# Performance work log

Hardware: AMD Instinct MI355X
Metric: run time of the kernel (lower is better)

## Reference

```python
import jax, jax.numpy as jnp
import numpy as np

N_NODES = 100000   # number of atoms in the (batched) molecular graph
N_EDGES = 1600000  # directed edges (avg degree 16)
F_DIM = 128        # featureSize
P_DIM = 2048       # fingerPrintLength
RADIUS = 4


def setup_inputs() -> dict:
    key = jax.random.key(0)
    k1, k2, k3, k4, k5 = jax.random.split(key, 5)
    atomsFeatures = jax.random.normal(k1, (N_NODES, F_DIM), dtype=jnp.float32)
    edge_src = jax.random.randint(k2, (N_EDGES,), 0, N_NODES, dtype=jnp.int32)
    edge_dst = jax.random.randint(k3, (N_EDGES,), 0, N_NODES, dtype=jnp.int32)
    W1 = jax.random.normal(k4, (F_DIM, F_DIM), dtype=jnp.float32) / np.float32(np.sqrt(F_DIM))
    b1 = jnp.zeros((F_DIM,), dtype=jnp.float32)
    W2 = jax.random.normal(k5, (F_DIM, P_DIM), dtype=jnp.float32) / np.float32(np.sqrt(F_DIM))
    b2 = jnp.zeros((P_DIM,), dtype=jnp.float32)
    return {"atomsFeatures": atomsFeatures, "W1": W1, "b1": b1,
            "W2": W2, "b2": b2, "edge_src": edge_src, "edge_dst": edge_dst}


def reference(atomsFeatures, W1, b1, W2, b2, edge_src, edge_dst):
    # Duvenaud neural fingerprint:
    # for r in range(radius):
    #   agg[i]  = x[i] + sum_{j in N(i)} x[j]          (gather + segment-sum)
    #   h       = relu(agg @ W1 + b1)                  (lin1)
    #   fp     += sum_i softmax(h @ W2 + b2)           (lin2 + softmax scatter-add)
    #   x       = h
    x = atomsFeatures
    fp = jnp.zeros((1, W2.shape[1]), dtype=x.dtype)
    for _ in range(RADIUS):
        neigh = jax.ops.segment_sum(x[edge_src], edge_dst, num_segments=N_NODES)
        agg = x + neigh                                    # [N, F]
        h = jax.nn.relu(agg @ W1 + b1)                     # [N, F]
        logits = h @ W2 + b2                               # [N, P]
        fp = fp + jnp.sum(jax.nn.softmax(logits, axis=-1), axis=0, keepdims=True)
        x = h
    return fp
```

## Files before the change

kernel.cpp:

```cpp
#include <hip/hip_runtime.h>
#include <hip/hip_bf16.h>
#include <cstdint>
#include <cstddef>

#define F_DIM 128
#define P_DIM 2048
#define RADIUS 4
#define HT_STRIDE 136
#define LOG2E 1.4426950408889634f

typedef short s16x8 __attribute__((ext_vector_type(8)));
typedef float f32x4 __attribute__((ext_vector_type(4)));
typedef float f32x2 __attribute__((ext_vector_type(2)));

static __device__ __forceinline__ float bf2f(ushort u) {
    union { float f; uint i; } v; v.i = ((uint)u) << 16; return v.f;
}
static __device__ __forceinline__ ushort f2bf(float f) {
    uint u = __float_as_uint(f);
    uint r = (u + 0x7fffu + ((u >> 16) & 1u)) >> 16;
    return (ushort)r;
}
static __device__ __forceinline__ f32x2 bfpair(uint u) {
    union { float f; uint i; } lo, hi;
    lo.i = u << 16; hi.i = u & 0xffff0000u;
    f32x2 r; r.x = lo.f; r.y = hi.f; return r;
}
static __device__ __forceinline__ f32x4 mfma16(s16x8 a, s16x8 b, f32x4 c) {
    return __builtin_amdgcn_mfma_f32_16x16x32_bf16(a, b, c, 0, 0, 0);
}
static __device__ __forceinline__ float ex2(float x) { return __builtin_amdgcn_exp2f(x); }
static __device__ __forceinline__ float lg2(float x) { return __builtin_amdgcn_logf(x); }


__global__ void hist_kernel(const int* __restrict__ dst, int* __restrict__ counts, int E) {
    int e = blockIdx.x * blockDim.x + threadIdx.x;
    if (e < E) atomicAdd(&counts[dst[e]], 1);
}

__global__ __launch_bounds__(1024) void scan1_kernel(const int* __restrict__ counts,
                                                     int* __restrict__ offs,
                                                     int* __restrict__ partials, int N) {
    __shared__ int buf[2][1024];
    int i = (blockIdx.x << 10) + threadIdx.x;
    int v = (i < N) ? counts[i] : 0;
    int src = 0;
    buf[0][threadIdx.x] = v;
    __syncthreads();
    for (int off = 1; off < 1024; off <<= 1) {
        int d = src ^ 1;
        int val = buf[src][threadIdx.x];
        if (threadIdx.x >= (unsigned)off) val += buf[src][threadIdx.x - off];
        buf[d][threadIdx.x] = val;
        src = d;
        __syncthreads();
    }
    int inc = buf[src][threadIdx.x];
    if (i < N) offs[i + 1] = inc;
    if (threadIdx.x == 1023) partials[blockIdx.x] = inc;
}

__global__ __launch_bounds__(1024) void scan2_kernel(int* __restrict__ partials, int nb) {
    __shared__ int buf[2][1024];
    int t = threadIdx.x;
    int v = (t < nb) ? partials[t] : 0;
    int src = 0;
    buf[0][t] = v;
    __syncthreads();
    for (int off = 1; off < 1024; off <<= 1) {
        int d = src ^ 1;
        int val = buf[src][t];
        if (t >= (unsigned)off) val += buf[src][t - off];
        buf[d][t] = val;
        src = d;
        __syncthreads();
    }
    if (t < nb) partials[t] = (t == 0) ? 0 : buf[src][t - 1];
}

__global__ void scan3_kernel(int* __restrict__ offs, const int* __restrict__ partials, int N) {
    int i = blockIdx.x * blockDim.x + threadIdx.x;
    if (i < N) offs[i + 1] += partials[i >> 10];
    if (i == 0) offs[0] = 0;
}

__global__ void copy_kernel(const int* __restrict__ offs, int* __restrict__ cursor, int N) {
    int i = blockIdx.x * blockDim.x + threadIdx.x;
    if (i < N) cursor[i] = offs[i];
}

__global__ void scatter_kernel(const int* __restrict__ src, const int* __restrict__ dst,
                               int* __restrict__ cursor, int* __restrict__ srcs_sorted, int E) {
    int e = blockIdx.x * blockDim.x + threadIdx.x;
    if (e < E) {
        int d = dst[e];
        int pos = atomicAdd(&cursor[d], 1);
        srcs_sorted[pos] = src[e];
    }
}


__global__ void cvt_bf16_kernel(const float* __restrict__ src, ushort* __restrict__ dst, int n) {
    int i = blockIdx.x * blockDim.x + threadIdx.x;
    if (i < n) dst[i] = f2bf(src[i]);
}

__global__ void scale_kernel(const float* __restrict__ src, float* __restrict__ dst,
                             int n, float scale) {
    int i = blockIdx.x * blockDim.x + threadIdx.x;
    if (i < n) dst[i] = src[i] * scale;
}

__global__ void swizzle_split_kernel(const float* __restrict__ src, ushort* __restrict__ dst,
                                     int P, int total, float scale) {
    int d = blockIdx.x * blockDim.x + threadIdx.x;
    if (d >= total) return;
    int j    = d & 7;
    int lane = (d >> 3) & 63;
    int s    = (d >> 9) & 1;
    int kt   = (d >> 10) & 3;
    int pt   = d >> 12;
    int k = kt * 32 + (lane >> 4) * 8 + j;
    int p = pt * 16 + (lane & 15);
    float w = src[k * P + p] * scale;
    ushort hi = f2bf(w);
    ushort out = hi;
    if (s) out = f2bf(w - bf2f(hi));
    dst[d] = out;
}


#define ACC8(acc2, u) { \
    acc2[0] += bfpair(u.x); acc2[1] += bfpair(u.y); \
    acc2[2] += bfpair(u.z); acc2[3] += bfpair(u.w); }

__global__ __launch_bounds__(256) void agg_kernel(const ushort* __restrict__ x,
                                                  const int* __restrict__ offs,
                                                  const int* __restrict__ srcs,
                                                  ushort* __restrict__ agg, int N) {
    int wid = (blockIdx.x * blockDim.x + threadIdx.x) >> 6;
    int lane = threadIdx.x & 63;
    int q = lane >> 4;
    int l16 = lane & 15;
    int n0 = wid * 8 + q;
    int n1 = wid * 8 + 4 + q;
    const uint4* xr = (const uint4*)x;

    f32x2 accA[4], accB[4];
    #pragma unroll
    for (int i = 0; i < 4; ++i) { accA[i] = (f32x2){0.f, 0.f}; accB[i] = (f32x2){0.f, 0.f}; }
    int eA = 0, eA1 = 0, eB = 0, eB1 = 0;
    if (n0 < N) {
        uint4 v = xr[(size_t)n0 * 16 + l16];
        ACC8(accA, v);
        eA = offs[n0]; eA1 = offs[n0 + 1];
    }
    if (n1 < N) {
        uint4 v = xr[(size_t)n1 * 16 + l16];
        ACC8(accB, v);
        eB = offs[n1]; eB1 = offs[n1 + 1];
    }
    while (eA + 2 <= eA1 && eB + 2 <= eB1) {
        int ja0 = srcs[eA], ja1 = srcs[eA + 1]; eA += 2;
        int jb0 = srcs[eB], jb1 = srcs[eB + 1]; eB += 2;
        uint4 ua0 = xr[(size_t)ja0 * 16 + l16];
        uint4 ua1 = xr[(size_t)ja1 * 16 + l16];
        uint4 ub0 = xr[(size_t)jb0 * 16 + l16];
        uint4 ub1 = xr[(size_t)jb1 * 16 + l16];
        ACC8(accA, ua0); ACC8(accA, ua1);
        ACC8(accB, ub0); ACC8(accB, ub1);
    }
    while (eA < eA1 && eB < eB1) {
        int ja = srcs[eA++];
        int jb = srcs[eB++];
        uint4 ua = xr[(size_t)ja * 16 + l16];
        uint4 ub = xr[(size_t)jb * 16 + l16];
        ACC8(accA, ua);
        ACC8(accB, ub);
    }
    while (eA < eA1) {
        int ja = srcs[eA++];
        uint4 ua = xr[(size_t)ja * 16 + l16];
        ACC8(accA, ua);
    }
    while (eB < eB1) {
        int jb = srcs[eB++];
        uint4 ub = xr[(size_t)jb * 16 + l16];
        ACC8(accB, ub);
    }
    if (n0 < N) {
        uint4 o;
        o.x = ((uint)f2bf(accA[0].y) << 16) | (uint)f2bf(accA[0].x);
        o.y = ((uint)f2bf(accA[1].y) << 16) | (uint)f2bf(accA[1].x);
        o.z = ((uint)f2bf(accA[2].y) << 16) | (uint)f2bf(accA[2].x);
        o.w = ((uint)f2bf(accA[3].y) << 16) | (uint)f2bf(accA[3].x);
        ((uint4*)agg)[(size_t)n0 * 16 + l16] = o;
    }
    if (n1 < N) {
        uint4 o;
        o.x = ((uint)f2bf(accB[0].y) << 16) | (uint)f2bf(accB[0].x);
        o.y = ((uint)f2bf(accB[1].y) << 16) | (uint)f2bf(accB[1].x);
        o.z = ((uint)f2bf(accB[2].y) << 16) | (uint)f2bf(accB[2].x);
        o.w = ((uint)f2bf(accB[3].y) << 16) | (uint)f2bf(accB[3].x);
        ((uint4*)agg)[(size_t)n1 * 16 + l16] = o;
    }
}


#define LOADB(bb_) { _Pragma("unroll") for (int f = 0; f < 8; ++f) bb_[f] = wpn[f * 64]; wpn += 512; }

#define MFMA4(cc, bb_) { \
    _Pragma("unroll") for (int g = 0; g < 4; ++g) cc[g] = mfma16(a[g][0], bb_[0], czero); \
    _Pragma("unroll") for (int g = 0; g < 4; ++g) cc[g] = mfma16(a[g][0], bb_[1], cc[g]); \
    _Pragma("unroll") for (int kt = 1; kt < 4; ++kt) { \
        _Pragma("unroll") for (int g = 0; g < 4; ++g) cc[g] = mfma16(a[g][kt], bb_[kt * 2 + 0], cc[g]); \
        _Pragma("unroll") for (int g = 0; g < 4; ++g) cc[g] = mfma16(a[g][kt], bb_[kt * 2 + 1], cc[g]); } }

#define P1_UPD4(cc, bbv) { \
    f32x2 bb2; bb2.x = (bbv); bb2.y = (bbv); \
    _Pragma("unroll") for (int g = 0; g < 4; ++g) \
    _Pragma("unroll") for (int h = 0; h < 2; ++h) { \
        int j2 = g * 2 + h; \
        f32x2 v; v.x = cc[g][2 * h]; v.y = cc[g][2 * h + 1]; \
        v = v + bb2; \
        f32x2 d = v - m2_[j2]; \
        f32x2 e; e.x = ex2(-fabsf(d.x)); e.y = ex2(-fabsf(d.y)); \
        f32x2 t1 = s2_[j2] + e; \
        f32x2 t2 = __builtin_elementwise_fma(s2_[j2], e, one2); \
        s2_[j2].x = d.x > 0.f ? t2.x : t1.x; \
        s2_[j2].y = d.y > 0.f ? t2.y : t1.y; \
        m2_[j2] = __builtin_elementwise_max(m2_[j2], v); \
    } }

#define P2_UPD4(cc, bbv, ptv) { \
    f32x2 bb2; bb2.x = (bbv); bb2.y = (bbv); \
    f32x2 tot2; tot2.x = 0.f; tot2.y = 0.f; \
    _Pragma("unroll") for (int g = 0; g < 4; ++g) \
    _Pragma("unroll") for (int h = 0; h < 2; ++h) { \
        f32x2 v; v.x = cc[g][2 * h]; v.y = cc[g][2 * h + 1]; \
        v = v + bb2 + bbk2[g * 2 + h]; \
        tot2.x += ex2(v.x); tot2.y += ex2(v.y); \
    } \
    float tot = tot2.x + tot2.y; \
    tot += __shfl_xor(tot, 16); \
    tot += __shfl_xor(tot, 32); \
    if (lane < 16) atomicAdd(&fp[(ptv) * 16 + lane], tot); }

__global__ __launch_bounds__(256, 2) void round_kernel(
        const ushort* __restrict__ agg,
        const ushort* __restrict__ w1sw,
        const float*  __restrict__ b1,
        const ushort* __restrict__ w2sw,
        const float*  __restrict__ b2l,
        ushort* __restrict__ h_out,
        float* __restrict__ fp,
        int N) {
    __shared__ ushort smem_u[64 * HT_STRIDE];
    ushort* hT = smem_u;
    float* mbuf = (float*)smem_u;
    float* sbuf = ((float*)smem_u) + 256;

    const int tid = threadIdx.x;
    const int w = tid >> 6;
    const int lane = tid & 63;
    const int q = lane >> 4;
    const int l15 = lane & 15;
    const int nodeBase = blockIdx.x * 64;
    const int ptBase = w * 32;

    const f32x4 czero = {0.f, 0.f, 0.f, 0.f};
    f32x2 one2; one2.x = 1.0f; one2.y = 1.0f;

    const s16x8* w1v = (const s16x8*)w1sw;
    const s16x8* w2v = (const s16x8*)w2sw;

    s16x8 a[4][4];
    #pragma unroll
    for (int g = 0; g < 4; ++g) {
        int node = nodeBase + g * 16 + l15;
        #pragma unroll
        for (int kt = 0; kt < 4; ++kt) {
            if (node < N)
                a[g][kt] = *(const s16x8*)(agg + (size_t)node * F_DIM + kt * 32 + q * 8);
            else
                a[g][kt] = (s16x8){0, 0, 0, 0, 0, 0, 0, 0};
        }
    }

    #pragma unroll
    for (int t = 0; t < 2; ++t) {
        int pt = 2 * w + t;
        f32x4 c[4];
        const s16x8* wp = w1v + pt * 8 * 64;
        {
            s16x8 bh = wp[0 * 64 + lane];
            s16x8 bl = wp[1 * 64 + lane];
            #pragma unroll
            for (int g = 0; g < 4; ++g) {
                c[g] = mfma16(a[g][0], bh, czero);
                c[g] = mfma16(a[g][0], bl, c[g]);
            }
        }
        #pragma unroll
        for (int kt = 1; kt < 4; ++kt) {
            s16x8 bh = wp[(kt * 2 + 0) * 64 + lane];
            s16x8 bl = wp[(kt * 2 + 1) * 64 + lane];
            #pragma unroll
            for (int g = 0; g < 4; ++g) {
                c[g] = mfma16(a[g][kt], bh, c[g]);
                c[g] = mfma16(a[g][kt], bl, c[g]);
            }
        }
        float bb = b1[pt * 16 + l15];
        #pragma unroll
        for (int g = 0; g < 4; ++g)
            #pragma unroll
            for (int r = 0; r < 4; ++r) {
                float v = c[g][r] + bb;
                v = v > 0.f ? v : 0.f;
                hT[(g * 16 + q * 4 + r) * HT_STRIDE + pt * 16 + l15] = f2bf(v);
            }
    }
    __syncthreads();

    #pragma unroll
    for (int it = 0; it < 4; ++it) {
        int idx = it * 256 + tid;
        int row = idx >> 4;
        int chunk = idx & 15;
        int gnode = nodeBase + row;
        if (gnode < N) {
            s16x8 vv = *(const s16x8*)&hT[row * HT_STRIDE + chunk * 8];
            *(s16x8*)(h_out + (size_t)gnode * F_DIM + chunk * 8) = vv;
        }
    }

    #pragma unroll
    for (int g = 0; g < 4; ++g)
        #pragma unroll
        for (int kt = 0; kt < 4; ++kt)
            a[g][kt] = *(const s16x8*)&hT[(g * 16 + l15) * HT_STRIDE + kt * 32 + q * 8];
    __syncthreads();

    f32x2 m2_[8], s2_[8];
    #pragma unroll
    for (int j = 0; j < 8; ++j) {
        m2_[j].x = -INFINITY; m2_[j].y = -INFINITY;
        s2_[j].x = 0.f;       s2_[j].y = 0.f;
    }

    {
        const s16x8* wpn = w2v + ptBase * 8 * 64 + lane;
        const float* bpn = b2l + ptBase * 16 + l15;
        s16x8 bA[8], bB[8];
        f32x4 cA[4], cB[4];
        float bbA, bbB;
        LOADB(bA); bbA = *bpn; bpn += 16;
        LOADB(bB); bbB = *bpn; bpn += 16;
        MFMA4(cA, bA);
        #pragma unroll 1
        for (int k = 0; k < 15; ++k) {
            float bbu = bbA;
            LOADB(bA); bbA = *bpn; bpn += 16;
            MFMA4(cB, bB);
            P1_UPD4(cA, bbu);
            float bbv = bbB;
            LOADB(bB); bbB = *bpn; bpn += 16;
            MFMA4(cA, bA);
            P1_UPD4(cB, bbv);
        }
        MFMA4(cB, bB);
        P1_UPD4(cA, bbA);
        P1_UPD4(cB, bbB);
    }

    #pragma unroll
    for (int j = 0; j < 16; ++j) {
        int j2 = (j >> 2) * 2 + ((j >> 1) & 1);
        int cmp = j & 1;
        float mm = m2_[j2][cmp], ss = s2_[j2][cmp];
        #pragma unroll
        for (int off = 1; off <= 8; off <<= 1) {
            float om = __shfl_xor(mm, off);
            float os = __shfl_xor(ss, off);
            float nm = fmaxf(mm, om);
            ss = ss * ex2(mm - nm) + os * ex2(om - nm);
            mm = nm;
        }
        if (l15 == 0) {
            int node = (j >> 2) * 16 + q * 4 + (j & 3);
            mbuf[node * 4 + w] = mm;
            sbuf[node * 4 + w] = ss;
        }
    }
    __syncthreads();

    f32x2 bbk2[8];
    #pragma unroll
    for (int j = 0; j < 16; ++j) {
        int node = (j >> 2) * 16 + q * 4 + (j & 3);
        float4 mv = *(const float4*)&mbuf[node * 4];
        float4 sv = *(const float4*)&sbuf[node * 4];
        float nm = fmaxf(fmaxf(mv.x, mv.y), fmaxf(mv.z, mv.w));
        float ss = sv.x * ex2(mv.x - nm) + sv.y * ex2(mv.y - nm)
                 + sv.z * ex2(mv.z - nm) + sv.w * ex2(mv.w - nm);
        float bb = (nodeBase + node < N) ? (-nm - lg2(ss)) : -INFINITY;
        int j2 = (j >> 2) * 2 + ((j >> 1) & 1);
        bbk2[j2][j & 1] = bb;
    }

    {
        const s16x8* wpn = w2v + ptBase * 8 * 64 + lane;
        const float* bpn = b2l + ptBase * 16 + l15;
        s16x8 bA[8], bB[8];
        f32x4 cA[4], cB[4];
        float bbA, bbB;
        LOADB(bA); bbA = *bpn; bpn += 16;
        LOADB(bB); bbB = *bpn; bpn += 16;
        MFMA4(cA, bA);
        #pragma unroll 1
        for (int k = 0; k < 15; ++k) {
            float bbu = bbA;
            LOADB(bA); bbA = *bpn; bpn += 16;
            MFMA4(cB, bB);
            P2_UPD4(cA, bbu, ptBase + 2 * k);
            float bbv = bbB;
            LOADB(bB); bbB = *bpn; bpn += 16;
            MFMA4(cA, bA);
            P2_UPD4(cB, bbv, ptBase + 2 * k + 1);
        }
        MFMA4(cB, bB);
        P2_UPD4(cA, bbA, ptBase + 30);
        P2_UPD4(cB, bbB, ptBase + 31);
    }
}


extern "C" void kernel_launch(void* const* d_in, const int* in_sizes, int n_in,
                              void* d_out, int out_size, void* d_ws, size_t ws_size,
                              hipStream_t stream) {
    const float* atoms = (const float*)d_in[0];
    const float* W1    = (const float*)d_in[1];
    const float* b1    = (const float*)d_in[2];
    const float* W2    = (const float*)d_in[3];
    const float* b2    = (const float*)d_in[4];
    const int* esrc    = (const int*)d_in[5];
    const int* edst    = (const int*)d_in[6];
    float* fp          = (float*)d_out;
    const int N = in_sizes[0] / F_DIM;
    const int E = in_sizes[5];

    char* ws = (char*)d_ws;
    ushort* xA   = (ushort*)ws;  ws += (size_t)N * F_DIM * sizeof(ushort);
    ushort* xB   = (ushort*)ws;  ws += (size_t)N * F_DIM * sizeof(ushort);
    ushort* aggb = (ushort*)ws;  ws += (size_t)N * F_DIM * sizeof(ushort);
    ushort* w1sw = (ushort*)ws;  ws += (size_t)F_DIM * F_DIM * 2 * sizeof(ushort);
    ushort* w2sw = (ushort*)ws;  ws += (size_t)F_DIM * P_DIM * 2 * sizeof(ushort);
    float*  b2l  = (float*)ws;   ws += (size_t)P_DIM * sizeof(float);
    int* offs    = (int*)ws;     ws += (((size_t)(N + 1) * sizeof(int) + 255) & ~255ull);
    int* cursor  = (int*)ws;     ws += (((size_t)N * sizeof(int) + 255) & ~255ull);
    int* partials = (int*)ws;    ws += 4096;
    int* srcs    = (int*)ws;

    hipMemsetAsync(d_out, 0, (size_t)out_size * sizeof(float), stream);
    hipMemsetAsync(cursor, 0, (size_t)N * sizeof(int), stream);

    int eb = (E + 255) / 256;
    hist_kernel<<<eb, 256, 0, stream>>>(edst, cursor, E);
    int nb1 = (N + 1023) >> 10;
    scan1_kernel<<<nb1, 1024, 0, stream>>>(cursor, offs, partials, N);
    scan2_kernel<<<1, 1024, 0, stream>>>(partials, nb1);
    scan3_kernel<<<(N + 255) / 256, 256, 0, stream>>>(offs, partials, N);
    copy_kernel<<<(N + 255) / 256, 256, 0, stream>>>(offs, cursor, N);
    scatter_kernel<<<eb, 256, 0, stream>>>(esrc, edst, cursor, srcs, E);

    int nconv = N * F_DIM;
    cvt_bf16_kernel<<<(nconv + 255) / 256, 256, 0, stream>>>(atoms, xA, nconv);
    int t1 = F_DIM * F_DIM * 2;
    swizzle_split_kernel<<<(t1 + 255) / 256, 256, 0, stream>>>(W1, w1sw, F_DIM, t1, 1.0f);
    int t2 = F_DIM * P_DIM * 2;
    swizzle_split_kernel<<<(t2 + 255) / 256, 256, 0, stream>>>(W2, w2sw, P_DIM, t2, LOG2E);
    scale_kernel<<<(P_DIM + 255) / 256, 256, 0, stream>>>(b2, b2l, P_DIM, LOG2E);

    const ushort* x = xA;
    ushort* xnext = xB;
    int rblocks = (N + 63) / 64;
    int ablocks = (N + 31) / 32;
    for (int r = 0; r < RADIUS; ++r) {
        agg_kernel<<<ablocks, 256, 0, stream>>>(x, offs, srcs, aggb, N);
        round_kernel<<<rblocks, 256, 0, stream>>>(aggb, w1sw, b1, w2sw, b2l,
                                                  xnext, fp, N);
        x = xnext;
        xnext = (xnext == xB) ? xA : xB;
    }
}
```

Measured before the change: 1.534 ms.

## Give each wave its own node rows across all P columns, dropping cross-wave softmax merge

The round kernel now assigns each wave 32 nodes over the full 2048-column output, instead of 64 nodes shared by four waves that each cover a quarter of the columns. Each wave's online-softmax stats are therefore complete, which removes the shared-memory max/sum exchange and two block barriers. Blocks grow to 128 nodes and periodic __syncthreads are added in the W2 loops, presumably to keep waves in step for cache reuse of W2. The trade-off is that each wave streams all of W2 twice, so per-wave W2 loads and atomicAdd traffic to fp rise four-fold.

```diff
diff --git a/kernel.cpp b/kernel.cpp
--- a/kernel.cpp
+++ b/kernel.cpp
@@ -209,16 +209,16 @@
 
 #define LOADB(bb_) { _Pragma("unroll") for (int f = 0; f < 8; ++f) bb_[f] = wpn[f * 64]; wpn += 512; }
 
-#define MFMA4(cc, bb_) { \
-    _Pragma("unroll") for (int g = 0; g < 4; ++g) cc[g] = mfma16(a[g][0], bb_[0], czero); \
-    _Pragma("unroll") for (int g = 0; g < 4; ++g) cc[g] = mfma16(a[g][0], bb_[1], cc[g]); \
+#define MFMA2(cc, bb_) { \
+    _Pragma("unroll") for (int g = 0; g < 2; ++g) cc[g] = mfma16(a[g][0], bb_[0], czero); \
+    _Pragma("unroll") for (int g = 0; g < 2; ++g) cc[g] = mfma16(a[g][0], bb_[1], cc[g]); \
     _Pragma("unroll") for (int kt = 1; kt < 4; ++kt) { \
-        _Pragma("unroll") for (int g = 0; g < 4; ++g) cc[g] = mfma16(a[g][kt], bb_[kt * 2 + 0], cc[g]); \
-        _Pragma("unroll") for (int g = 0; g < 4; ++g) cc[g] = mfma16(a[g][kt], bb_[kt * 2 + 1], cc[g]); } }
-
-#define P1_UPD4(cc, bbv) { \
+        _Pragma("unroll") for (int g = 0; g < 2; ++g) cc[g] = mfma16(a[g][kt], bb_[kt * 2 + 0], cc[g]); \
+        _Pragma("unroll") for (int g = 0; g < 2; ++g) cc[g] = mfma16(a[g][kt], bb_[kt * 2 + 1], cc[g]); } }
+
+#define P1_UPD2(cc, bbv) { \
     f32x2 bb2; bb2.x = (bbv); bb2.y = (bbv); \
-    _Pragma("unroll") for (int g = 0; g < 4; ++g) \
+    _Pragma("unroll") for (int g = 0; g < 2; ++g) \
     _Pragma("unroll") for (int h = 0; h < 2; ++h) { \
         int j2 = g * 2 + h; \
         f32x2 v; v.x = cc[g][2 * h]; v.y = cc[g][2 * h + 1]; \
@@ -232,10 +232,10 @@
         m2_[j2] = __builtin_elementwise_max(m2_[j2], v); \
     } }
 
-#define P2_UPD4(cc, bbv, ptv) { \
+#define P2_UPD2(cc, bbv, ptv) { \
     f32x2 bb2; bb2.x = (bbv); bb2.y = (bbv); \
     f32x2 tot2; tot2.x = 0.f; tot2.y = 0.f; \
-    _Pragma("unroll") for (int g = 0; g < 4; ++g) \
+    _Pragma("unroll") for (int g = 0; g < 2; ++g) \
     _Pragma("unroll") for (int h = 0; h < 2; ++h) { \
         f32x2 v; v.x = cc[g][2 * h]; v.y = cc[g][2 * h + 1]; \
         v = v + bb2 + bbk2[g * 2 + h]; \
@@ -255,18 +255,15 @@
         ushort* __restrict__ h_out,
         float* __restrict__ fp,
         int N) {
-    __shared__ ushort smem_u[64 * HT_STRIDE];
-    ushort* hT = smem_u;
-    float* mbuf = (float*)smem_u;
-    float* sbuf = ((float*)smem_u) + 256;
+    __shared__ ushort hT[128 * HT_STRIDE];
 
     const int tid = threadIdx.x;
     const int w = tid >> 6;
     const int lane = tid & 63;
     const int q = lane >> 4;
     const int l15 = lane & 15;
-    const int nodeBase = blockIdx.x * 64;
-    const int ptBase = w * 32;
+    const int nodeBase = blockIdx.x * 128;
+    const int rowBase = w * 32;
 
     const f32x4 czero = {0.f, 0.f, 0.f, 0.f};
     f32x2 one2; one2.x = 1.0f; one2.y = 1.0f;
@@ -274,10 +271,10 @@
     const s16x8* w1v = (const s16x8*)w1sw;
     const s16x8* w2v = (const s16x8*)w2sw;
 
-    s16x8 a[4][4];
-    #pragma unroll
-    for (int g = 0; g < 4; ++g) {
-        int node = nodeBase + g * 16 + l15;
+    s16x8 a[2][4];
+    #pragma unroll
+    for (int g = 0; g < 2; ++g) {
+        int node = nodeBase + rowBase + g * 16 + l15;
         #pragma unroll
         for (int kt = 0; kt < 4; ++kt) {
             if (node < N)
@@ -287,16 +284,15 @@
         }
     }
 
-    #pragma unroll
-    for (int t = 0; t < 2; ++t) {
-        int pt = 2 * w + t;
-        f32x4 c[4];
-        const s16x8* wp = w1v + pt * 8 * 64;
+    #pragma unroll 1
+    for (int ft = 0; ft < 8; ++ft) {
+        f32x4 c[2];
+        const s16x8* wp = w1v + ft * 8 * 64;
         {
             s16x8 bh = wp[0 * 64 + lane];
             s16x8 bl = wp[1 * 64 + lane];
             #pragma unroll
-            for (int g = 0; g < 4; ++g) {
+            for (int g = 0; g < 2; ++g) {
                 c[g] = mfma16(a[g][0], bh, czero);
                 c[g] = mfma16(a[g][0], bl, c[g]);
             }
@@ -306,76 +302,76 @@
             s16x8 bh = wp[(kt * 2 + 0) * 64 + lane];
             s16x8 bl = wp[(kt * 2 + 1) * 64 + lane];
             #pragma unroll
-            for (int g = 0; g < 4; ++g) {
+            for (int g = 0; g < 2; ++g) {
                 c[g] = mfma16(a[g][kt], bh, c[g]);
                 c[g] = mfma16(a[g][kt], bl, c[g]);
             }
         }
-        float bb = b1[pt * 16 + l15];
+        float bb = b1[ft * 16 + l15];
         #pragma unroll
-        for (int g = 0; g < 4; ++g)
+        for (int g = 0; g < 2; ++g)
             #pragma unroll
             for (int r = 0; r < 4; ++r) {
                 float v = c[g][r] + bb;
                 v = v > 0.f ? v : 0.f;
-                hT[(g * 16 + q * 4 + r) * HT_STRIDE + pt * 16 + l15] = f2bf(v);
+                hT[(rowBase + g * 16 + q * 4 + r) * HT_STRIDE + ft * 16 + l15] = f2bf(v);
             }
     }
-    __syncthreads();
-
-    #pragma unroll
-    for (int it = 0; it < 4; ++it) {
-        int idx = it * 256 + tid;
+
+    #pragma unroll
+    for (int it = 0; it < 8; ++it) {
+        int idx = it * 64 + lane;
         int row = idx >> 4;
         int chunk = idx & 15;
-        int gnode = nodeBase + row;
+        int gnode = nodeBase + rowBase + row;
         if (gnode < N) {
-            s16x8 vv = *(const s16x8*)&hT[row * HT_STRIDE + chunk * 8];
+            s16x8 vv = *(const s16x8*)&hT[(rowBase + row) * HT_STRIDE + chunk * 8];
             *(s16x8*)(h_out + (size_t)gnode * F_DIM + chunk * 8) = vv;
         }
     }
 
     #pragma unroll
-    for (int g = 0; g < 4; ++g)
+    for (int g = 0; g < 2; ++g)
         #pragma unroll
         for (int kt = 0; kt < 4; ++kt)
-            a[g][kt] = *(const s16x8*)&hT[(g * 16 + l15) * HT_STRIDE + kt * 32 + q * 8];
-    __syncthreads();
-
-    f32x2 m2_[8], s2_[8];
-    #pragma unroll
-    for (int j = 0; j < 8; ++j) {
+            a[g][kt] = *(const s16x8*)&hT[(rowBase + g * 16 + l15) * HT_STRIDE + kt * 32 + q * 8];
+
+    f32x2 m2_[4], s2_[4];
+    #pragma unroll
+    for (int j = 0; j < 4; ++j) {
         m2_[j].x = -INFINITY; m2_[j].y = -INFINITY;
         s2_[j].x = 0.f;       s2_[j].y = 0.f;
     }
 
     {
-        const s16x8* wpn = w2v + ptBase * 8 * 64 + lane;
-        const float* bpn = b2l + ptBase * 16 + l15;
+        const s16x8* wpn = w2v + lane;
+        const float* bpn = b2l + l15;
         s16x8 bA[8], bB[8];
-        f32x4 cA[4], cB[4];
+        f32x4 cA[2], cB[2];
         float bbA, bbB;
         LOADB(bA); bbA = *bpn; bpn += 16;
         LOADB(bB); bbB = *bpn; bpn += 16;
-        MFMA4(cA, bA);
+        MFMA2(cA, bA);
         #pragma unroll 1
-        for (int k = 0; k < 15; ++k) {
+        for (int k = 0; k < 63; ++k) {
             float bbu = bbA;
             LOADB(bA); bbA = *bpn; bpn += 16;
-            MFMA4(cB, bB);
-            P1_UPD4(cA, bbu);
+            MFMA2(cB, bB);
+            P1_UPD2(cA, bbu);
             float bbv = bbB;
             LOADB(bB); bbB = *bpn; bpn += 16;
-            MFMA4(cA, bA);
-            P1_UPD4(cB, bbv);
-        }
-        MFMA4(cB, bB);
-        P1_UPD4(cA, bbA);
-        P1_UPD4(cB, bbB);
-    }
-
-    #pragma unroll
-    for (int j = 0; j < 16; ++j) {
+            MFMA2(cA, bA);
+            P1_UPD2(cB, bbv);
+            if ((k & 3) == 3) __syncthreads();
+        }
+        MFMA2(cB, bB);
+        P1_UPD2(cA, bbA);
+        P1_UPD2(cB, bbB);
+    }
+
+    f32x2 bbk2[4];
+    #pragma unroll
+    for (int j = 0; j < 8; ++j) {
         int j2 = (j >> 2) * 2 + ((j >> 1) & 1);
         int cmp = j & 1;
         float mm = m2_[j2][cmp], ss = s2_[j2][cmp];
@@ -387,51 +383,34 @@
             ss = ss * ex2(mm - nm) + os * ex2(om - nm);
             mm = nm;
         }
-        if (l15 == 0) {
-            int node = (j >> 2) * 16 + q * 4 + (j & 3);
-            mbuf[node * 4 + w] = mm;
-            sbuf[node * 4 + w] = ss;
-        }
-    }
-    __syncthreads();
-
-    f32x2 bbk2[8];
-    #pragma unroll
-    for (int j = 0; j < 16; ++j) {
-        int node = (j >> 2) * 16 + q * 4 + (j & 3);
-        float4 mv = *(const float4*)&mbuf[node * 4];
-        float4 sv = *(const float4*)&sbuf[node * 4];
-        float nm = fmaxf(fmaxf(mv.x, mv.y), fmaxf(mv.z, mv.w));
-        float ss = sv.x * ex2(mv.x - nm) + sv.y * ex2(mv.y - nm)
-                 + sv.z * ex2(mv.z - nm) + sv.w * ex2(mv.w - nm);
-        float bb = (nodeBase + node < N) ? (-nm - lg2(ss)) : -INFINITY;
-        int j2 = (j >> 2) * 2 + ((j >> 1) & 1);
-        bbk2[j2][j & 1] = bb;
+        int node = nodeBase + rowBase + (j >> 2) * 16 + q * 4 + (j & 3);
+        bbk2[j2][cmp] = (node < N) ? (-mm - lg2(ss)) : -INFINITY;
     }
 
     {
-        const s16x8* wpn = w2v + ptBase * 8 * 64 + lane;
-        const float* bpn = b2l + ptBase * 16 + l15;
+        const s16x8* wpn = w2v + lane;
+        const float* bpn = b2l + l15;
         s16x8 bA[8], bB[8];
-        f32x4 cA[4], cB[4];
+        f32x4 cA[2], cB[2];
         float bbA, bbB;
         LOADB(bA); bbA = *bpn; bpn += 16;
         LOADB(bB); bbB = *bpn; bpn += 16;
-        MFMA4(cA, bA);
+        MFMA2(cA, bA);
         #pragma unroll 1
-        for (int k = 0; k < 15; ++k) {
+        for (int k = 0; k < 63; ++k) {
             float bbu = bbA;
             LOADB(bA); bbA = *bpn; bpn += 16;
-            MFMA4(cB, bB);
-            P2_UPD4(cA, bbu, ptBase + 2 * k);
+            MFMA2(cB, bB);
+            P2_UPD2(cA, bbu, 2 * k);
             float bbv = bbB;
             LOADB(bB); bbB = *bpn; bpn += 16;
-            MFMA4(cA, bA);
-            P2_UPD4(cB, bbv, ptBase + 2 * k + 1);
-        }
-        MFMA4(cB, bB);
-        P2_UPD4(cA, bbA, ptBase + 30);
-        P2_UPD4(cB, bbB, ptBase + 31);
+            MFMA2(cA, bA);
+            P2_UPD2(cB, bbv, 2 * k + 1);
+            if ((k & 3) == 3) __syncthreads();
+        }
+        MFMA2(cB, bB);
+        P2_UPD2(cA, bbA, 126);
+        P2_UPD2(cB, bbB, 127);
     }
 }
 
@@ -484,7 +463,7 @@
 
     const ushort* x = xA;
     ushort* xnext = xB;
-    int rblocks = (N + 63) / 64;
+    int rblocks = (N + 127) / 128;
     int ablocks = (N + 31) / 32;
     for (int r = 0; r < RADIUS; ++r) {
         agg_kernel<<<ablocks, 256, 0, stream>>>(x, offs, srcs, aggb, N);
```

After: 1.994 ms. +30.0%, slower.
